# Kernel tuning notes

Hardware: AMD Instinct MI355X
Metric: run time of the kernel (lower is better)

Reference implementation:

```python
import jax, jax.numpy as jnp
from jax import lax
import numpy as np

N = 10                      # spline knots
STEP = 1.0 / (N - 1)
B, E, NC, H, W = 64, 2, 8, 256, 256

def _interp_matrix(n, step):
    # natural-cubic-spline second-derivative solve matrix (constant, numpy at trace time)
    mat = 4.0 * np.eye(n - 2)
    np.fill_diagonal(mat[1:, :-1], 1.0)
    np.fill_diagonal(mat[:-1, 1:], 1.0)
    A = 6.0 * np.linalg.inv(mat) / step ** 2
    z = np.zeros(n - 2)
    A = np.vstack([z, A, z])
    Bm = np.zeros([n - 2, n])
    np.fill_diagonal(Bm, 1.0)
    np.fill_diagonal(Bm[:, 1:], -2.0)
    np.fill_diagonal(Bm[:, 2:], 1.0)
    return (A @ Bm).astype(np.float32)

MAT = jnp.asarray(_interp_matrix(N, STEP))  # (N, N)


def setup_inputs() -> dict:
    key = jax.random.key(0)
    ks = iter(jax.random.split(key, 40))
    def w(shape, scale=0.05):
        return jax.random.normal(next(ks), shape, jnp.float32) * scale
    d = {"batch": jax.random.uniform(next(ks), (B, 3, H, W), jnp.float32)}
    chans = [3, NC, 2 * NC, 4 * NC, 8 * NC, 16 * NC]
    for i in range(1, 6):
        d[f"w{i}"] = w((chans[i], chans[i - 1], 3, 3))
        d[f"bias{i}"] = jnp.zeros((chans[i],), jnp.float32)
    for i in range(2, 6):
        c = chans[i]
        d[f"bn{i}_gamma"] = jnp.ones((c,), jnp.float32)
        d[f"bn{i}_beta"] = jnp.zeros((c,), jnp.float32)
        d[f"bn{i}_mean"] = jnp.zeros((c,), jnp.float32)
        d[f"bn{i}_var"] = jnp.ones((c,), jnp.float32)
    d["l1_w"] = w((16 * NC, 16 * NC))
    d["l1_b"] = jnp.zeros((16 * NC,), jnp.float32)
    d["l2_w"] = w((3 * N * E, 16 * NC))
    d["l2_b"] = jnp.zeros((3 * N * E,), jnp.float32)
    return d


def _conv(x, w, b):
    y = lax.conv_general_dilated(x, w, (2, 2), 'VALID',
                                 dimension_numbers=('NCHW', 'OIHW', 'NCHW'))
    return y + b[None, :, None, None]


def _bn(x, g, beta, m, v):
    s = (g * lax.rsqrt(v + 1e-5))
    return (x - m[None, :, None, None]) * s[None, :, None, None] + beta[None, :, None, None]


def _coeffs(yt):
    # yt: (B, E, 3, N) knot values (ys + identity). Returns a,b,c,d each (B,E,3,N-1).
    M = jnp.einsum('ij,becj->beci', MAT, yt)
    h = STEP
    a = (M[..., 1:] - M[..., :-1]) / (6.0 * h)
    b = M[..., :-1] / 2.0
    c = (yt[..., 1:] - yt[..., :-1]) / h - (M[..., 1:] + 2.0 * M[..., :-1]) * (h / 6.0)
    d = yt[..., :-1]
    return a, b, c, d


def _apply(a, b, c, d, xi, xf):
    # a..d: (B,E,3,N-1); xi int (B,E,3,P); xf float broadcastable to (B,E,3,P)
    ga = jnp.take_along_axis(a, xi, axis=-1)
    gb = jnp.take_along_axis(b, xi, axis=-1)
    gc = jnp.take_along_axis(c, xi, axis=-1)
    gd = jnp.take_along_axis(d, xi, axis=-1)
    return ((ga * xf + gb) * xf + gc) * xf + gd


def reference(batch, w1, bias1, w2, bias2, w3, bias3, w4, bias4, w5, bias5,
              bn2_gamma, bn2_beta, bn2_mean, bn2_var,
              bn3_gamma, bn3_beta, bn3_mean, bn3_var,
              bn4_gamma, bn4_beta, bn4_mean, bn4_var,
              bn5_gamma, bn5_beta, bn5_mean, bn5_var,
              l1_w, l1_b, l2_w, l2_b):
    y = jax.nn.relu(_conv(batch, w1, bias1))
    y = _bn(jax.nn.relu(_conv(y, w2, bias2)), bn2_gamma, bn2_beta, bn2_mean, bn2_var)
    y = _bn(jax.nn.relu(_conv(y, w3, bias3)), bn3_gamma, bn3_beta, bn3_mean, bn3_var)
    y = _bn(jax.nn.relu(_conv(y, w4, bias4)), bn4_gamma, bn4_beta, bn4_mean, bn4_var)
    y = _bn(jax.nn.relu(_conv(y, w5, bias5)), bn5_gamma, bn5_beta, bn5_mean, bn5_var)
    feat = jnp.mean(y, axis=(2, 3))                      # AvgPool2d(7) on 7x7 -> (B, 16*NC)
    hh = jax.nn.relu(feat @ l1_w.T + l1_b)
    ys = (hh @ l2_w.T + l2_b).reshape(B, E, 3, N)        # per-expert per-channel knot residuals
    identity = (jnp.arange(N, dtype=jnp.float32) / (N - 1))
    yt = ys + identity                                   # residual curves around identity
    a, b, c, d = _coeffs(yt)                             # each (B,E,3,N-1)

    # per-pixel bucketize + coefficient gather + cubic Horner eval
    P = H * W
    xv = batch.reshape(B, 3, P)
    xi = jnp.clip(jnp.floor(xv / STEP), 0, N - 2).astype(jnp.int32)
    xf = (xv - xi.astype(jnp.float32) * STEP)[:, None, :, :]       # (B,1,3,P)
    idx = jnp.broadcast_to(xi[:, None, :, :], (B, E, 3, P))
    out = _apply(a, b, c, d, idx, xf)                              # (B,E,3,P)
    out = out.reshape(B, E, 3, H, W).transpose(1, 0, 2, 3, 4)      # (E,B,3,H,W)

    # sampled spline curves over 255 uniform values
    vals = jnp.arange(0.0, 1.0, 1.0 / 255, dtype=jnp.float32)      # (255,)
    V = vals.shape[0]
    vi = jnp.clip(jnp.floor(vals / STEP), 0, N - 2).astype(jnp.int32)
    vf = vals - vi.astype(jnp.float32) * STEP
    vidx = jnp.broadcast_to(vi[None, None, None, :], (B, E, 3, V))
    splines = _apply(a, b, c, d, vidx, vf[None, None, None, :])    # (B,E,3,V)
    splines = splines.transpose(1, 0, 2, 3)                        # (E,B,3,V)
    return out, splines
```

## Files before the change

### kernel.cpp

```cpp
#include <hip/hip_runtime.h>
#include <hip/hip_bf16.h>

#define STEP_F (1.0f/9.0f)

typedef float f4 __attribute__((ext_vector_type(4)));

__global__ __launch_bounds__(256) void conv1_k(const float* __restrict__ x,
                                               const float* __restrict__ w,
                                               const float* __restrict__ bias,
                                               float* __restrict__ y)
{
    int idx = blockIdx.x * 256 + threadIdx.x;
    int owg = idx & 31;
    int t1  = idx >> 5;
    int oh  = t1 % 127;
    int b   = t1 / 127;
    int iw0 = owg * 8;
    int ih0 = oh * 2;
    const float* xb = x + (size_t)b * 3 * 65536;

    float acc[8][4];
    #pragma unroll
    for (int c = 0; c < 8; ++c)
        #pragma unroll
        for (int t = 0; t < 4; ++t) acc[c][t] = 0.0f;

    #pragma unroll
    for (int ci = 0; ci < 3; ++ci) {
        float r[3][10];
        #pragma unroll
        for (int kh = 0; kh < 3; ++kh) {
            const float* row = xb + ci * 65536 + (ih0 + kh) * 256;
            #pragma unroll
            for (int t = 0; t < 5; ++t) {
                int c = iw0 + 2 * t; if (c > 254) c = 254;
                float2 v = *(const float2*)(row + c);
                r[kh][2*t] = v.x; r[kh][2*t+1] = v.y;
            }
        }
        #pragma unroll
        for (int co = 0; co < 8; ++co) {
            float wr[9];
            #pragma unroll
            for (int k = 0; k < 9; ++k) wr[k] = w[(co * 3 + ci) * 9 + k];
            #pragma unroll
            for (int t = 0; t < 4; ++t) {
                float a = acc[co][t];
                #pragma unroll
                for (int kh = 0; kh < 3; ++kh)
                    a = fmaf(r[kh][2*t+0], wr[kh*3+0],
                        fmaf(r[kh][2*t+1], wr[kh*3+1],
                        fmaf(r[kh][2*t+2], wr[kh*3+2], a)));
                acc[co][t] = a;
            }
        }
    }
    int ow0 = owg * 4;
    #pragma unroll
    for (int co = 0; co < 8; ++co) {
        float bs = bias[co];
        float4 o;
        o.x = fmaxf(acc[co][0] + bs, 0.0f);
        o.y = fmaxf(acc[co][1] + bs, 0.0f);
        o.z = fmaxf(acc[co][2] + bs, 0.0f);
        o.w = fmaxf(acc[co][3] + bs, 0.0f);
        *(float4*)(y + (((size_t)b * 8 + co) * 127 + oh) * 128 + ow0) = o;
    }
}

__global__ __launch_bounds__(256) void conv2_k(
    const float* __restrict__ x,
    const float* __restrict__ w, const float* __restrict__ bias,
    const float* __restrict__ g, const float* __restrict__ be,
    const float* __restrict__ mn, const float* __restrict__ vr,
    float* __restrict__ y)
{
    __shared__ float lds[8 * 9 * 128 + 192];
    const int b   = blockIdx.x;
    const int ohg = blockIdx.y;
    const int oh0 = ohg * 4;
    const int ih0 = oh0 * 2;
    const int tid = threadIdx.x;

    {
        const int col = tid & 127;
        const int rp  = tid >> 7;
        const int rows = (127 - ih0) < 9 ? (127 - ih0) : 9;
        #pragma unroll
        for (int ci = 0; ci < 8; ++ci) {
            const float* gp = x + (((size_t)b * 8 + ci) * 127 + ih0) * 128 + col;
            float* lp = lds + ci * 1152 + col;
            for (int rr = rp; rr < rows; rr += 2)
                lp[rr * 128] = gp[rr * 128];
        }
    }
    __syncthreads();

    const int lane = tid & 63;
    const int wv   = __builtin_amdgcn_readfirstlane(tid >> 6);
    const int ow   = lane;
    const int co0  = wv * 4;

    float acc[4][4];
    #pragma unroll
    for (int c = 0; c < 4; ++c)
        #pragma unroll
        for (int j = 0; j < 4; ++j) acc[c][j] = 0.0f;

    #pragma unroll 2
    for (int ci = 0; ci < 8; ++ci) {
        float wr[4][9];
        #pragma unroll
        for (int c = 0; c < 4; ++c) {
            const int wb = __builtin_amdgcn_readfirstlane(((co0 + c) * 8 + ci) * 9);
            #pragma unroll
            for (int k = 0; k < 9; ++k) wr[c][k] = w[wb + k];
        }
        const float* lci = lds + ci * 1152;
        #pragma unroll
        for (int r = 0; r < 9; ++r) {
            float2 x01 = *(const float2*)&lci[r * 128 + 2 * ow];
            float  x2  = lci[r * 128 + 2 * ow + 2];
            #pragma unroll
            for (int kh = 0; kh < 3; ++kh) {
                const int jj = r - kh;
                if (jj >= 0 && (jj & 1) == 0 && (jj >> 1) < 4) {
                    const int j = jj >> 1;
                    #pragma unroll
                    for (int c = 0; c < 4; ++c)
                        acc[c][j] = fmaf(x01.x, wr[c][kh*3+0],
                                    fmaf(x01.y, wr[c][kh*3+1],
                                    fmaf(x2,    wr[c][kh*3+2], acc[c][j])));
                }
            }
        }
    }

    if (ow < 63) {
        #pragma unroll
        for (int c = 0; c < 4; ++c) {
            const int co = co0 + c;
            const float bs = bias[co];
            const float s  = g[co] / sqrtf(vr[co] + 1e-5f);
            const float sh = be[co] - mn[co] * s;
            #pragma unroll
            for (int j = 0; j < 4; ++j) {
                int oh = oh0 + j;
                if (oh < 63)
                    y[(((size_t)b * 16 + co) * 63 + oh) * 64 + ow] =
                        fmaxf(acc[c][j] + bs, 0.0f) * s + sh;
            }
        }
    }
}

__global__ __launch_bounds__(256) void conv3_k(
    const float* __restrict__ x,
    const float* __restrict__ w, const float* __restrict__ bias,
    const float* __restrict__ g, const float* __restrict__ be,
    const float* __restrict__ mn, const float* __restrict__ vr,
    float* __restrict__ y)
{
    const int b   = blockIdx.x;
    const int ohg = blockIdx.y;
    const int coh = blockIdx.z;
    const int lane = threadIdx.x & 63;
    const int wv   = __builtin_amdgcn_readfirstlane(threadIdx.x >> 6);
    const int ow   = lane & 31;
    const int ohl  = lane >> 5;
    const int co0  = coh * 16 + wv * 4;
    const int ihb  = ohg * 8 + ohl * 4;

    float acc[4][2];
    #pragma unroll
    for (int c = 0; c < 4; ++c) { acc[c][0] = 0.0f; acc[c][1] = 0.0f; }

    #pragma unroll 4
    for (int ci = 0; ci < 16; ++ci) {
        const float* gp = x + (((size_t)b * 16 + ci) * 63) * 64 + 2 * ow;
        f4 rv[5];
        #pragma unroll
        for (int r = 0; r < 5; ++r) {
            int ih = ihb + r; ih = ih > 62 ? 62 : ih;
            rv[r] = *(const f4*)(gp + ih * 64);
        }
        float wr[4][9];
        #pragma unroll
        for (int c = 0; c < 4; ++c) {
            const int wb = __builtin_amdgcn_readfirstlane(((co0 + c) * 16 + ci) * 9);
            #pragma unroll
            for (int k = 0; k < 9; ++k) wr[c][k] = w[wb + k];
        }
        #pragma unroll
        for (int j = 0; j < 2; ++j)
            #pragma unroll
            for (int kh = 0; kh < 3; ++kh) {
                const f4 v = rv[2*j + kh];
                #pragma unroll
                for (int c = 0; c < 4; ++c)
                    acc[c][j] = fmaf(v[0], wr[c][kh*3+0],
                                fmaf(v[1], wr[c][kh*3+1],
                                fmaf(v[2], wr[c][kh*3+2], acc[c][j])));
            }
    }

    if (ow < 31) {
        #pragma unroll
        for (int c = 0; c < 4; ++c) {
            const int co = co0 + c;
            const float bs = bias[co];
            const float s  = g[co] / sqrtf(vr[co] + 1e-5f);
            const float sh = be[co] - mn[co] * s;
            #pragma unroll
            for (int j = 0; j < 2; ++j) {
                int oh = ohg * 4 + ohl * 2 + j;
                if (oh < 31)
                    y[(((size_t)b * 32 + co) * 31 + oh) * 32 + ow] =
                        fmaxf(acc[c][j] + bs, 0.0f) * s + sh;
            }
        }
    }
}

__global__ __launch_bounds__(256) void conv4_k(
    const float* __restrict__ x,
    const float* __restrict__ w, const float* __restrict__ bias,
    const float* __restrict__ g, const float* __restrict__ be,
    const float* __restrict__ mn, const float* __restrict__ vr,
    float* __restrict__ y)
{
    const int b   = blockIdx.x;
    const int ohg = blockIdx.y;
    const int cog = blockIdx.z;
    const int lane = threadIdx.x & 63;
    const int wv   = __builtin_amdgcn_readfirstlane(threadIdx.x >> 6);
    const int ow   = lane & 15;
    const int ohl  = lane >> 4;
    const int oh   = ohg * 4 + ohl;
    const int co0  = cog * 16 + wv * 4;
    const int ihb  = 2 * oh;

    float acc[4];
    #pragma unroll
    for (int c = 0; c < 4; ++c) acc[c] = 0.0f;

    #pragma unroll 4
    for (int ci = 0; ci < 32; ++ci) {
        const float* gp = x + (((size_t)b * 32 + ci) * 31) * 32 + 2 * ow;
        f4 rv[3];
        #pragma unroll
        for (int r = 0; r < 3; ++r) {
            int ih = ihb + r; ih = ih > 30 ? 30 : ih;
            rv[r] = *(const f4*)(gp + ih * 32);
        }
        float wr[4][9];
        #pragma unroll
        for (int c = 0; c < 4; ++c) {
            const int wb = __builtin_amdgcn_readfirstlane(((co0 + c) * 32 + ci) * 9);
            #pragma unroll
            for (int k = 0; k < 9; ++k) wr[c][k] = w[wb + k];
        }
        #pragma unroll
        for (int kh = 0; kh < 3; ++kh) {
            const f4 v = rv[kh];
            #pragma unroll
            for (int c = 0; c < 4; ++c)
                acc[c] = fmaf(v[0], wr[c][kh*3+0],
                         fmaf(v[1], wr[c][kh*3+1],
                         fmaf(v[2], wr[c][kh*3+2], acc[c])));
        }
    }

    if (ow < 15 && oh < 15) {
        #pragma unroll
        for (int c = 0; c < 4; ++c) {
            const int co = co0 + c;
            const float bs = bias[co];
            const float s  = g[co] / sqrtf(vr[co] + 1e-5f);
            const float sh = be[co] - mn[co] * s;
            y[(((size_t)b * 64 + co) * 15 + oh) * 16 + ow] =
                fmaxf(acc[c] + bs, 0.0f) * s + sh;
        }
    }
}

__global__ __launch_bounds__(256) void conv5m_k(
    const float* __restrict__ x,
    const float* __restrict__ w, const float* __restrict__ bias,
    const float* __restrict__ g, const float* __restrict__ be,
    const float* __restrict__ mn, const float* __restrict__ vr,
    float* __restrict__ feat)
{
    __shared__ float red[2048];
    const int b    = blockIdx.x;
    const int co0  = blockIdx.y * 8;
    const int tid  = threadIdx.x;
    const int wv   = __builtin_amdgcn_readfirstlane(tid >> 6);
    const int lane = tid & 63;
    const int pr = lane >> 3, pc = lane & 7;

    float acc[8];
    #pragma unroll
    for (int c = 0; c < 8; ++c) acc[c] = 0.0f;

    #pragma unroll 4
    for (int i = 0; i < 16; ++i) {
        const int ci = wv * 16 + i;
        const float* gp = x + (((size_t)b * 64 + ci) * 15) * 16 + 2 * pc;
        f4 rv[3];
        #pragma unroll
        for (int r = 0; r < 3; ++r) {
            int ih = 2 * pr + r; ih = ih > 14 ? 14 : ih;
            rv[r] = *(const f4*)(gp + ih * 16);
        }
        float wr[8][9];
        #pragma unroll
        for (int c = 0; c < 8; ++c) {
            const int wb = __builtin_amdgcn_readfirstlane(((co0 + c) * 64 + ci) * 9);
            #pragma unroll
            for (int k = 0; k < 9; ++k) wr[c][k] = w[wb + k];
        }
        #pragma unroll
        for (int kh = 0; kh < 3; ++kh) {
            const f4 v = rv[kh];
            #pragma unroll
            for (int c = 0; c < 8; ++c)
                acc[c] = fmaf(v[0], wr[c][kh*3+0],
                         fmaf(v[1], wr[c][kh*3+1],
                         fmaf(v[2], wr[c][kh*3+2], acc[c])));
        }
    }

    #pragma unroll
    for (int c = 0; c < 8; ++c) red[wv * 512 + lane * 8 + c] = acc[c];
    __syncthreads();
    if (wv == 0) {
        const bool act = (pr < 7) && (pc < 7);
        #pragma unroll
        for (int c = 0; c < 8; ++c) {
            float v = red[lane*8+c] + red[512+lane*8+c]
                    + red[1024+lane*8+c] + red[1536+lane*8+c];
            const int co = co0 + c;
            const float s  = g[co] / sqrtf(vr[co] + 1e-5f);
            v = fmaxf(v + bias[co], 0.0f) * s + (be[co] - mn[co] * s);
            v = act ? v : 0.0f;
            #pragma unroll
            for (int off = 32; off; off >>= 1) v += __shfl_xor(v, off, 64);
            if (lane == 0) feat[(size_t)b * 128 + co] = v * (1.0f / 49.0f);
        }
    }
}

__global__ __launch_bounds__(256) void tail_k(
    const float* __restrict__ featg, const float* __restrict__ l1w,
    const float* __restrict__ l1b, const float* __restrict__ l2w,
    const float* __restrict__ l2b, float* __restrict__ coef,
    float* __restrict__ spl)
{
    __shared__ float feat[128];
    __shared__ float hh[128];
    __shared__ float ysv[64];
    __shared__ float cfl[216];
    const int b = blockIdx.x, t = threadIdx.x;

    if (t < 128) feat[t] = featg[(size_t)b * 128 + t];
    __syncthreads();
    if (t < 128) {
        const float4* wp = (const float4*)(l1w + (size_t)t * 128);
        float s = l1b[t];
        #pragma unroll 8
        for (int k = 0; k < 32; ++k) {
            float4 v = wp[k];
            s += v.x*feat[4*k] + v.y*feat[4*k+1] + v.z*feat[4*k+2] + v.w*feat[4*k+3];
        }
        hh[t] = fmaxf(s, 0.0f);
    }
    __syncthreads();
    if (t < 60) {
        const float4* wp = (const float4*)(l2w + (size_t)t * 128);
        float s = l2b[t];
        #pragma unroll 8
        for (int k = 0; k < 32; ++k) {
            float4 v = wp[k];
            s += v.x*hh[4*k] + v.y*hh[4*k+1] + v.z*hh[4*k+2] + v.w*hh[4*k+3];
        }
        ysv[t] = s;
    }
    __syncthreads();
    if (t < 6) {
        const float h = STEP_F;
        float yt[10];
        #pragma unroll
        for (int n = 0; n < 10; ++n) yt[n] = ysv[t * 10 + n] + (float)n * h;
        float r[8];
        const float k6h2 = 6.0f / (h * h);
        #pragma unroll
        for (int i = 0; i < 8; ++i) r[i] = k6h2 * (yt[i] - 2.0f * yt[i+1] + yt[i+2]);
        float cp[8], dp[8];
        cp[0] = 0.25f; dp[0] = r[0] * 0.25f;
        #pragma unroll
        for (int i = 1; i < 8; ++i) {
            float m = 4.0f - cp[i-1];
            cp[i] = 1.0f / m;
            dp[i] = (r[i] - dp[i-1]) / m;
        }
        float M[10];
        M[0] = 0.0f; M[9] = 0.0f; M[8] = dp[7];
        #pragma unroll
        for (int i = 6; i >= 0; --i) M[i+1] = dp[i] - cp[i] * M[i+2];
        float* cg = coef + ((size_t)b * 6 + t) * 36;
        #pragma unroll
        for (int i = 0; i < 9; ++i) {
            float ca = (M[i+1] - M[i]) / (6.0f * h);
            float cb = M[i] * 0.5f;
            float cc = (yt[i+1] - yt[i]) / h - (M[i+1] + 2.0f * M[i]) * (h / 6.0f);
            float cd = yt[i];
            cfl[t*36 + i]      = ca;  cg[i]      = ca;
            cfl[t*36 + 9 + i]  = cb;  cg[9 + i]  = cb;
            cfl[t*36 + 18 + i] = cc;  cg[18 + i] = cc;
            cfl[t*36 + 27 + i] = cd;  cg[27 + i] = cd;
        }
    }
    __syncthreads();
    for (int i = t; i < 1530; i += 256) {
        int v = i % 255, ec = i / 255;
        float val = (float)v * (1.0f / 255.0f);
        int vi = (int)floorf(val / STEP_F);
        vi = vi < 0 ? 0 : (vi > 8 ? 8 : vi);
        float vf = val - (float)vi * STEP_F;
        const float* c = cfl + ec * 36;
        int e = ec / 3, ch = ec % 3;
        spl[(((size_t)e * 64 + b) * 3 + ch) * 255 + v] =
            ((c[vi]*vf + c[9+vi])*vf + c[18+vi])*vf + c[27+vi];
    }
}

__global__ __launch_bounds__(256) void apply2_k(const float* __restrict__ batch,
                                                const float* __restrict__ coef,
                                                float* __restrict__ out)
{
    int bc = blockIdx.y;
    int b = bc / 3, ch = bc % 3;
    int lane = threadIdx.x & 63;
    int j = lane < 9 ? lane : 8;
    const float* c0p = coef + ((size_t)(b * 6 + 0 + ch)) * 36;
    const float* c1p = coef + ((size_t)(b * 6 + 3 + ch)) * 36;
    float A0 = c0p[j], B0 = c0p[9 + j], C0 = c0p[18 + j], D0 = c0p[27 + j];
    float A1 = c1p[j], B1 = c1p[9 + j], C1 = c1p[18 + j], D1 = c1p[27 + j];

    const int P = 65536;
    size_t base = ((size_t)b * 3 + ch) * P;
    int p0 = (blockIdx.x * blockDim.x + threadIdx.x) * 4;

    float4 xv = *(const float4*)(batch + base + p0);
    float xs[4] = {xv.x, xv.y, xv.z, xv.w};
    float r0[4], r1[4];
    #pragma unroll
    for (int k = 0; k < 4; ++k) {
        float x = xs[k];
        int xi = (int)floorf(x / STEP_F);
        xi = xi < 0 ? 0 : (xi > 8 ? 8 : xi);
        float xf = x - (float)xi * STEP_F;
        int bidx = xi << 2;
        float ga0 = __int_as_float(__builtin_amdgcn_ds_bpermute(bidx, __float_as_int(A0)));
        float gb0 = __int_as_float(__builtin_amdgcn_ds_bpermute(bidx, __float_as_int(B0)));
        float gc0 = __int_as_float(__builtin_amdgcn_ds_bpermute(bidx, __float_as_int(C0)));
        float gd0 = __int_as_float(__builtin_amdgcn_ds_bpermute(bidx, __float_as_int(D0)));
        float ga1 = __int_as_float(__builtin_amdgcn_ds_bpermute(bidx, __float_as_int(A1)));
        float gb1 = __int_as_float(__builtin_amdgcn_ds_bpermute(bidx, __float_as_int(B1)));
        float gc1 = __int_as_float(__builtin_amdgcn_ds_bpermute(bidx, __float_as_int(C1)));
        float gd1 = __int_as_float(__builtin_amdgcn_ds_bpermute(bidx, __float_as_int(D1)));
        r0[k] = fmaf(fmaf(fmaf(ga0, xf, gb0), xf, gc0), xf, gd0);
        r1[k] = fmaf(fmaf(fmaf(ga1, xf, gb1), xf, gc1), xf, gd1);
    }
    float4 o0 = {r0[0], r0[1], r0[2], r0[3]};
    float4 o1 = {r1[0], r1[1], r1[2], r1[3]};
    size_t off0 = (((size_t)0 * 64 + b) * 3 + ch) * P + p0;
    size_t off1 = (((size_t)1 * 64 + b) * 3 + ch) * P + p0;
    *(float4*)(out + off0) = o0;
    *(float4*)(out + off1) = o1;
}

extern "C" void kernel_launch(void* const* d_in, const int* in_sizes, int n_in,
                              void* d_out, int out_size, void* d_ws, size_t ws_size,
                              hipStream_t stream) {
    const float* batch = (const float*)d_in[0];
    const float* w1 = (const float*)d_in[1];  const float* b1 = (const float*)d_in[2];
    const float* w2 = (const float*)d_in[3];  const float* b2 = (const float*)d_in[4];
    const float* w3 = (const float*)d_in[5];  const float* b3 = (const float*)d_in[6];
    const float* w4 = (const float*)d_in[7];  const float* b4 = (const float*)d_in[8];
    const float* w5 = (const float*)d_in[9];  const float* b5 = (const float*)d_in[10];
    const float* bn2g = (const float*)d_in[11]; const float* bn2b = (const float*)d_in[12];
    const float* bn2m = (const float*)d_in[13]; const float* bn2v = (const float*)d_in[14];
    const float* bn3g = (const float*)d_in[15]; const float* bn3b = (const float*)d_in[16];
    const float* bn3m = (const float*)d_in[17]; const float* bn3v = (const float*)d_in[18];
    const float* bn4g = (const float*)d_in[19]; const float* bn4b = (const float*)d_in[20];
    const float* bn4m = (const float*)d_in[21]; const float* bn4v = (const float*)d_in[22];
    const float* bn5g = (const float*)d_in[23]; const float* bn5b = (const float*)d_in[24];
    const float* bn5m = (const float*)d_in[25]; const float* bn5v = (const float*)d_in[26];
    const float* l1w = (const float*)d_in[27]; const float* l1b = (const float*)d_in[28];
    const float* l2w = (const float*)d_in[29]; const float* l2b = (const float*)d_in[30];

    float* outp = (float*)d_out;
    float* y1 = outp;
    float* y2 = y1 + 8323072;
    float* y3 = y2 + 4128768;
    float* y4 = y3 + 2031616;

    float* coef  = (float*)d_ws;
    float* featw = coef + 13824;

    const int TPB = 256;
    conv1_k<<<1016, TPB, 0, stream>>>(batch, w1, b1, y1);
    conv2_k<<<dim3(64, 16), TPB, 0, stream>>>(y1, w2, b2, bn2g, bn2b, bn2m, bn2v, y2);
    conv3_k<<<dim3(64, 8, 2), TPB, 0, stream>>>(y2, w3, b3, bn3g, bn3b, bn3m, bn3v, y3);
    conv4_k<<<dim3(64, 4, 4), TPB, 0, stream>>>(y3, w4, b4, bn4g, bn4b, bn4m, bn4v, y4);
    conv5m_k<<<dim3(64, 16), TPB, 0, stream>>>(y4, w5, b5, bn5g, bn5b, bn5m, bn5v, featw);
    tail_k<<<64, TPB, 0, stream>>>(featw, l1w, l1b, l2w, l2b, coef, outp + 25165824);
    {
        dim3 grid(64, 192);
        apply2_k<<<grid, TPB, 0, stream>>>(batch, coef, outp);
    }
}
```

Baseline: 134.2 us.

## Fuse conv1 into conv2 via LDS tile and process two images per block in conv3-5

Conv1 is now computed per block directly into a shared-memory tile that conv2 consumes, removing the y1 global write and readback and one launch. Conv3, conv4 and conv5 each handle two batch images per block, halving grid size and reusing the loaded weights across both images. This trades the recomputation of overlapping conv1 halo rows and higher register pressure for lower memory traffic and fewer weight loads.

```diff
diff --git a/kernel.cpp b/kernel.cpp
--- a/kernel.cpp
+++ b/kernel.cpp
@@ -5,163 +5,146 @@
 
 typedef float f4 __attribute__((ext_vector_type(4)));
 
-__global__ __launch_bounds__(256) void conv1_k(const float* __restrict__ x,
-                                               const float* __restrict__ w,
-                                               const float* __restrict__ bias,
-                                               float* __restrict__ y)
+__global__ __launch_bounds__(256) void conv12_k(
+    const float* __restrict__ x,
+    const float* __restrict__ w1c, const float* __restrict__ b1c,
+    const float* __restrict__ w2c, const float* __restrict__ b2c,
+    const float* __restrict__ g, const float* __restrict__ be,
+    const float* __restrict__ mn, const float* __restrict__ vr,
+    float* __restrict__ y2)
 {
-    int idx = blockIdx.x * 256 + threadIdx.x;
-    int owg = idx & 31;
-    int t1  = idx >> 5;
-    int oh  = t1 % 127;
-    int b   = t1 / 127;
-    int iw0 = owg * 8;
-    int ih0 = oh * 2;
-    const float* xb = x + (size_t)b * 3 * 65536;
-
-    float acc[8][4];
-    #pragma unroll
-    for (int c = 0; c < 8; ++c)
-        #pragma unroll
-        for (int t = 0; t < 4; ++t) acc[c][t] = 0.0f;
-
-    #pragma unroll
-    for (int ci = 0; ci < 3; ++ci) {
-        float r[3][10];
-        #pragma unroll
-        for (int kh = 0; kh < 3; ++kh) {
-            const float* row = xb + ci * 65536 + (ih0 + kh) * 256;
-            #pragma unroll
-            for (int t = 0; t < 5; ++t) {
-                int c = iw0 + 2 * t; if (c > 254) c = 254;
-                float2 v = *(const float2*)(row + c);
-                r[kh][2*t] = v.x; r[kh][2*t+1] = v.y;
-            }
-        }
-        #pragma unroll
-        for (int co = 0; co < 8; ++co) {
-            float wr[9];
-            #pragma unroll
-            for (int k = 0; k < 9; ++k) wr[k] = w[(co * 3 + ci) * 9 + k];
-            #pragma unroll
-            for (int t = 0; t < 4; ++t) {
-                float a = acc[co][t];
-                #pragma unroll
-                for (int kh = 0; kh < 3; ++kh)
-                    a = fmaf(r[kh][2*t+0], wr[kh*3+0],
-                        fmaf(r[kh][2*t+1], wr[kh*3+1],
-                        fmaf(r[kh][2*t+2], wr[kh*3+2], a)));
-                acc[co][t] = a;
-            }
-        }
-    }
-    int ow0 = owg * 4;
-    #pragma unroll
-    for (int co = 0; co < 8; ++co) {
-        float bs = bias[co];
-        float4 o;
-        o.x = fmaxf(acc[co][0] + bs, 0.0f);
-        o.y = fmaxf(acc[co][1] + bs, 0.0f);
-        o.z = fmaxf(acc[co][2] + bs, 0.0f);
-        o.w = fmaxf(acc[co][3] + bs, 0.0f);
-        *(float4*)(y + (((size_t)b * 8 + co) * 127 + oh) * 128 + ow0) = o;
-    }
-}
-
-__global__ __launch_bounds__(256) void conv2_k(
+    __shared__ float y1t[8 * 1188 + 16];
+    const int b    = blockIdx.x;
+    const int ohg  = blockIdx.y;
+    const int tid  = threadIdx.x;
+    const int rows = (127 - 8 * ohg) < 9 ? (127 - 8 * ohg) : 9;
+
+    {
+        const int owg = tid & 31;
+        const int rg  = tid >> 5;
+        const float* xb = x + (size_t)b * 3 * 65536;
+        for (int r = rg; r < rows; r += 8) {
+            const int r1  = 8 * ohg + r;
+            const int ih0 = 2 * r1;
+            const int iw0 = owg * 8;
+            float acc1[8][4];
+            #pragma unroll
+            for (int c = 0; c < 8; ++c)
+                #pragma unroll
+                for (int t = 0; t < 4; ++t) acc1[c][t] = 0.0f;
+
+            #pragma unroll
+            for (int ci = 0; ci < 3; ++ci) {
+                float rr[3][10];
+                #pragma unroll
+                for (int kh = 0; kh < 3; ++kh) {
+                    const float* row = xb + ci * 65536 + (ih0 + kh) * 256;
+                    #pragma unroll
+                    for (int t = 0; t < 5; ++t) {
+                        int c = iw0 + 2 * t; if (c > 254) c = 254;
+                        float2 v = *(const float2*)(row + c);
+                        rr[kh][2*t] = v.x; rr[kh][2*t+1] = v.y;
+                    }
+                }
+                #pragma unroll
+                for (int co = 0; co < 8; ++co) {
+                    float wr[9];
+                    #pragma unroll
+                    for (int k = 0; k < 9; ++k) wr[k] = w1c[(co * 3 + ci) * 9 + k];
+                    #pragma unroll
+                    for (int t = 0; t < 4; ++t) {
+                        float a = acc1[co][t];
+                        #pragma unroll
+                        for (int kh = 0; kh < 3; ++kh)
+                            a = fmaf(rr[kh][2*t+0], wr[kh*3+0],
+                                fmaf(rr[kh][2*t+1], wr[kh*3+1],
+                                fmaf(rr[kh][2*t+2], wr[kh*3+2], a)));
+                        acc1[co][t] = a;
+                    }
+                }
+            }
+            #pragma unroll
+            for (int co = 0; co < 8; ++co) {
+                float bs = b1c[co];
+                f4 o;
+                o[0] = fmaxf(acc1[co][0] + bs, 0.0f);
+                o[1] = fmaxf(acc1[co][1] + bs, 0.0f);
+                o[2] = fmaxf(acc1[co][2] + bs, 0.0f);
+                o[3] = fmaxf(acc1[co][3] + bs, 0.0f);
+                *(f4*)&y1t[co * 1188 + r * 132 + owg * 4] = o;
+            }
+        }
+    }
+    __syncthreads();
+
+    {
+        const int lane = tid & 63;
+        const int wv   = __builtin_amdgcn_readfirstlane(tid >> 6);
+        const int ow   = lane;
+        const int co0  = wv * 4;
+
+        float acc[4][4];
+        #pragma unroll
+        for (int c = 0; c < 4; ++c)
+            #pragma unroll
+            for (int j = 0; j < 4; ++j) acc[c][j] = 0.0f;
+
+        #pragma unroll 2
+        for (int ci = 0; ci < 8; ++ci) {
+            float wr[4][9];
+            #pragma unroll
+            for (int c = 0; c < 4; ++c) {
+                const int wb = __builtin_amdgcn_readfirstlane(((co0 + c) * 8 + ci) * 9);
+                #pragma unroll
+                for (int k = 0; k < 9; ++k) wr[c][k] = w2c[wb + k];
+            }
+            const float* lci = y1t + ci * 1188;
+            #pragma unroll
+            for (int r = 0; r < 9; ++r) {
+                float2 x01 = *(const float2*)&lci[r * 132 + 2 * ow];
+                float  x2  = lci[r * 132 + 2 * ow + 2];
+                #pragma unroll
+                for (int kh = 0; kh < 3; ++kh) {
+                    const int jj = r - kh;
+                    if (jj >= 0 && (jj & 1) == 0 && (jj >> 1) < 4) {
+                        const int j = jj >> 1;
+                        #pragma unroll
+                        for (int c = 0; c < 4; ++c)
+                            acc[c][j] = fmaf(x01.x, wr[c][kh*3+0],
+                                        fmaf(x01.y, wr[c][kh*3+1],
+                                        fmaf(x2,    wr[c][kh*3+2], acc[c][j])));
+                    }
+                }
+            }
+        }
+
+        if (ow < 63) {
+            #pragma unroll
+            for (int c = 0; c < 4; ++c) {
+                const int co = co0 + c;
+                const float bs = b2c[co];
+                const float s  = g[co] / sqrtf(vr[co] + 1e-5f);
+                const float sh = be[co] - mn[co] * s;
+                #pragma unroll
+                for (int j = 0; j < 4; ++j) {
+                    int oh = 4 * ohg + j;
+                    if (oh < 63)
+                        y2[(((size_t)b * 16 + co) * 63 + oh) * 64 + ow] =
+                            fmaxf(acc[c][j] + bs, 0.0f) * s + sh;
+                }
+            }
+        }
+    }
+}
+
+__global__ __launch_bounds__(256) void conv3b_k(
     const float* __restrict__ x,
     const float* __restrict__ w, const float* __restrict__ bias,
     const float* __restrict__ g, const float* __restrict__ be,
     const float* __restrict__ mn, const float* __restrict__ vr,
     float* __restrict__ y)
 {
-    __shared__ float lds[8 * 9 * 128 + 192];
-    const int b   = blockIdx.x;
-    const int ohg = blockIdx.y;
-    const int oh0 = ohg * 4;
-    const int ih0 = oh0 * 2;
-    const int tid = threadIdx.x;
-
-    {
-        const int col = tid & 127;
-        const int rp  = tid >> 7;
-        const int rows = (127 - ih0) < 9 ? (127 - ih0) : 9;
-        #pragma unroll
-        for (int ci = 0; ci < 8; ++ci) {
-            const float* gp = x + (((size_t)b * 8 + ci) * 127 + ih0) * 128 + col;
-            float* lp = lds + ci * 1152 + col;
-            for (int rr = rp; rr < rows; rr += 2)
-                lp[rr * 128] = gp[rr * 128];
-        }
-    }
-    __syncthreads();
-
-    const int lane = tid & 63;
-    const int wv   = __builtin_amdgcn_readfirstlane(tid >> 6);
-    const int ow   = lane;
-    const int co0  = wv * 4;
-
-    float acc[4][4];
-    #pragma unroll
-    for (int c = 0; c < 4; ++c)
-        #pragma unroll
-        for (int j = 0; j < 4; ++j) acc[c][j] = 0.0f;
-
-    #pragma unroll 2
-    for (int ci = 0; ci < 8; ++ci) {
-        float wr[4][9];
-        #pragma unroll
-        for (int c = 0; c < 4; ++c) {
-            const int wb = __builtin_amdgcn_readfirstlane(((co0 + c) * 8 + ci) * 9);
-            #pragma unroll
-            for (int k = 0; k < 9; ++k) wr[c][k] = w[wb + k];
-        }
-        const float* lci = lds + ci * 1152;
-        #pragma unroll
-        for (int r = 0; r < 9; ++r) {
-            float2 x01 = *(const float2*)&lci[r * 128 + 2 * ow];
-            float  x2  = lci[r * 128 + 2 * ow + 2];
-            #pragma unroll
-            for (int kh = 0; kh < 3; ++kh) {
-                const int jj = r - kh;
-                if (jj >= 0 && (jj & 1) == 0 && (jj >> 1) < 4) {
-                    const int j = jj >> 1;
-                    #pragma unroll
-                    for (int c = 0; c < 4; ++c)
-                        acc[c][j] = fmaf(x01.x, wr[c][kh*3+0],
-                                    fmaf(x01.y, wr[c][kh*3+1],
-                                    fmaf(x2,    wr[c][kh*3+2], acc[c][j])));
-                }
-            }
-        }
-    }
-
-    if (ow < 63) {
-        #pragma unroll
-        for (int c = 0; c < 4; ++c) {
-            const int co = co0 + c;
-            const float bs = bias[co];
-            const float s  = g[co] / sqrtf(vr[co] + 1e-5f);
-            const float sh = be[co] - mn[co] * s;
-            #pragma unroll
-            for (int j = 0; j < 4; ++j) {
-                int oh = oh0 + j;
-                if (oh < 63)
-                    y[(((size_t)b * 16 + co) * 63 + oh) * 64 + ow] =
-                        fmaxf(acc[c][j] + bs, 0.0f) * s + sh;
-            }
-        }
-    }
-}
-
-__global__ __launch_bounds__(256) void conv3_k(
-    const float* __restrict__ x,
-    const float* __restrict__ w, const float* __restrict__ bias,
-    const float* __restrict__ g, const float* __restrict__ be,
-    const float* __restrict__ mn, const float* __restrict__ vr,
-    float* __restrict__ y)
-{
-    const int b   = blockIdx.x;
+    const int b0  = blockIdx.x, b1 = b0 + 32;
     const int ohg = blockIdx.y;
     const int coh = blockIdx.z;
     const int lane = threadIdx.x & 63;
@@ -171,18 +154,22 @@
     const int co0  = coh * 16 + wv * 4;
     const int ihb  = ohg * 8 + ohl * 4;
 
-    float acc[4][2];
+    float acc[2][4][2];
     #pragma unroll
-    for (int c = 0; c < 4; ++c) { acc[c][0] = 0.0f; acc[c][1] = 0.0f; }
-
-    #pragma unroll 4
+    for (int p = 0; p < 2; ++p)
+        #pragma unroll
+        for (int c = 0; c < 4; ++c) { acc[p][c][0] = 0.0f; acc[p][c][1] = 0.0f; }
+
+    #pragma unroll 2
     for (int ci = 0; ci < 16; ++ci) {
-        const float* gp = x + (((size_t)b * 16 + ci) * 63) * 64 + 2 * ow;
-        f4 rv[5];
+        const float* gp0 = x + (((size_t)b0 * 16 + ci) * 63) * 64 + 2 * ow;
+        const float* gp1 = x + (((size_t)b1 * 16 + ci) * 63) * 64 + 2 * ow;
+        f4 rv0[5], rv1[5];
         #pragma unroll
         for (int r = 0; r < 5; ++r) {
             int ih = ihb + r; ih = ih > 62 ? 62 : ih;
-            rv[r] = *(const f4*)(gp + ih * 64);
+            rv0[r] = *(const f4*)(gp0 + ih * 64);
+            rv1[r] = *(const f4*)(gp1 + ih * 64);
         }
         float wr[4][9];
         #pragma unroll
@@ -195,12 +182,17 @@
         for (int j = 0; j < 2; ++j)
             #pragma unroll
             for (int kh = 0; kh < 3; ++kh) {
-                const f4 v = rv[2*j + kh];
-                #pragma unroll
-                for (int c = 0; c < 4; ++c)
-                    acc[c][j] = fmaf(v[0], wr[c][kh*3+0],
-                                fmaf(v[1], wr[c][kh*3+1],
-                                fmaf(v[2], wr[c][kh*3+2], acc[c][j])));
+                const f4 v0 = rv0[2*j + kh];
+                const f4 v1 = rv1[2*j + kh];
+                #pragma unroll
+                for (int c = 0; c < 4; ++c) {
+                    acc[0][c][j] = fmaf(v0[0], wr[c][kh*3+0],
+                                   fmaf(v0[1], wr[c][kh*3+1],
+                                   fmaf(v0[2], wr[c][kh*3+2], acc[0][c][j])));
+                    acc[1][c][j] = fmaf(v1[0], wr[c][kh*3+0],
+                                   fmaf(v1[1], wr[c][kh*3+1],
+                                   fmaf(v1[2], wr[c][kh*3+2], acc[1][c][j])));
+                }
             }
     }
 
@@ -214,22 +206,25 @@
             #pragma unroll
             for (int j = 0; j < 2; ++j) {
                 int oh = ohg * 4 + ohl * 2 + j;
-                if (oh < 31)
-                    y[(((size_t)b * 32 + co) * 31 + oh) * 32 + ow] =
-                        fmaxf(acc[c][j] + bs, 0.0f) * s + sh;
-            }
-        }
-    }
-}
-
-__global__ __launch_bounds__(256) void conv4_k(
+                if (oh < 31) {
+                    y[(((size_t)b0 * 32 + co) * 31 + oh) * 32 + ow] =
+                        fmaxf(acc[0][c][j] + bs, 0.0f) * s + sh;
+                    y[(((size_t)b1 * 32 + co) * 31 + oh) * 32 + ow] =
+                        fmaxf(acc[1][c][j] + bs, 0.0f) * s + sh;
+                }
+            }
+        }
+    }
+}
+
+__global__ __launch_bounds__(256) void conv4b_k(
     const float* __restrict__ x,
     const float* __restrict__ w, const float* __restrict__ bias,
     const float* __restrict__ g, const float* __restrict__ be,
     const float* __restrict__ mn, const float* __restrict__ vr,
     float* __restrict__ y)
 {
-    const int b   = blockIdx.x;
+    const int b0  = blockIdx.x, b1 = b0 + 32;
     const int ohg = blockIdx.y;
     const int cog = blockIdx.z;
     const int lane = threadIdx.x & 63;
@@ -240,18 +235,22 @@
     const int co0  = cog * 16 + wv * 4;
     const int ihb  = 2 * oh;
 
-    float acc[4];
+    float acc[2][4];
     #pragma unroll
-    for (int c = 0; c < 4; ++c) acc[c] = 0.0f;
+    for (int p = 0; p < 2; ++p)
+        #pragma unroll
+        for (int c = 0; c < 4; ++c) acc[p][c] = 0.0f;
 
     #pragma unroll 4
     for (int ci = 0; ci < 32; ++ci) {
-        const float* gp = x + (((size_t)b * 32 + ci) * 31) * 32 + 2 * ow;
-        f4 rv[3];
+        const float* gp0 = x + (((size_t)b0 * 32 + ci) * 31) * 32 + 2 * ow;
+        const float* gp1 = x + (((size_t)b1 * 32 + ci) * 31) * 32 + 2 * ow;
+        f4 rv0[3], rv1[3];
         #pragma unroll
         for (int r = 0; r < 3; ++r) {
             int ih = ihb + r; ih = ih > 30 ? 30 : ih;
-            rv[r] = *(const f4*)(gp + ih * 32);
+            rv0[r] = *(const f4*)(gp0 + ih * 32);
+            rv1[r] = *(const f4*)(gp1 + ih * 32);
         }
         float wr[4][9];
         #pragma unroll
@@ -262,12 +261,17 @@
         }
         #pragma unroll
         for (int kh = 0; kh < 3; ++kh) {
-            const f4 v = rv[kh];
-            #pragma unroll
-            for (int c = 0; c < 4; ++c)
-                acc[c] = fmaf(v[0], wr[c][kh*3+0],
-                         fmaf(v[1], wr[c][kh*3+1],
-                         fmaf(v[2], wr[c][kh*3+2], acc[c])));
+            const f4 v0 = rv0[kh];
+            const f4 v1 = rv1[kh];
+            #pragma unroll
+            for (int c = 0; c < 4; ++c) {
+                acc[0][c] = fmaf(v0[0], wr[c][kh*3+0],
+                            fmaf(v0[1], wr[c][kh*3+1],
+                            fmaf(v0[2], wr[c][kh*3+2], acc[0][c])));
+                acc[1][c] = fmaf(v1[0], wr[c][kh*3+0],
+                            fmaf(v1[1], wr[c][kh*3+1],
+                            fmaf(v1[2], wr[c][kh*3+2], acc[1][c])));
+            }
         }
     }
 
@@ -278,40 +282,44 @@
             const float bs = bias[co];
             const float s  = g[co] / sqrtf(vr[co] + 1e-5f);
             const float sh = be[co] - mn[co] * s;
-            y[(((size_t)b * 64 + co) * 15 + oh) * 16 + ow] =
-                fmaxf(acc[c] + bs, 0.0f) * s + sh;
-        }
-    }
-}
-
-__global__ __launch_bounds__(256) void conv5m_k(
+            y[(((size_t)b0 * 64 + co) * 15 + oh) * 16 + ow] =
+                fmaxf(acc[0][c] + bs, 0.0f) * s + sh;
+            y[(((size_t)b1 * 64 + co) * 15 + oh) * 16 + ow] =
+                fmaxf(acc[1][c] + bs, 0.0f) * s + sh;
+        }
+    }
+}
+
+__global__ __launch_bounds__(256) void conv5m2_k(
     const float* __restrict__ x,
     const float* __restrict__ w, const float* __restrict__ bias,
     const float* __restrict__ g, const float* __restrict__ be,
     const float* __restrict__ mn, const float* __restrict__ vr,
     float* __restrict__ feat)
 {
-    __shared__ float red[2048];
-    const int b    = blockIdx.x;
+    __shared__ float red[2 * 2304 + 32];
+    const int b0   = blockIdx.x, b1 = b0 + 32;
     const int co0  = blockIdx.y * 8;
     const int tid  = threadIdx.x;
     const int wv   = __builtin_amdgcn_readfirstlane(tid >> 6);
     const int lane = tid & 63;
     const int pr = lane >> 3, pc = lane & 7;
 
-    float acc[8];
+    float a0[8], a1[8];
     #pragma unroll
-    for (int c = 0; c < 8; ++c) acc[c] = 0.0f;
+    for (int c = 0; c < 8; ++c) { a0[c] = 0.0f; a1[c] = 0.0f; }
 
     #pragma unroll 4
     for (int i = 0; i < 16; ++i) {
         const int ci = wv * 16 + i;
-        const float* gp = x + (((size_t)b * 64 + ci) * 15) * 16 + 2 * pc;
-        f4 rv[3];
+        const float* gp0 = x + (((size_t)b0 * 64 + ci) * 15) * 16 + 2 * pc;
+        const float* gp1 = x + (((size_t)b1 * 64 + ci) * 15) * 16 + 2 * pc;
+        f4 rv0[3], rv1[3];
         #pragma unroll
         for (int r = 0; r < 3; ++r) {
             int ih = 2 * pr + r; ih = ih > 14 ? 14 : ih;
-            rv[r] = *(const f4*)(gp + ih * 16);
+            rv0[r] = *(const f4*)(gp0 + ih * 16);
+            rv1[r] = *(const f4*)(gp1 + ih * 16);
         }
         float wr[8][9];
         #pragma unroll
@@ -322,31 +330,41 @@
         }
         #pragma unroll
         for (int kh = 0; kh < 3; ++kh) {
-            const f4 v = rv[kh];
-            #pragma unroll
-            for (int c = 0; c < 8; ++c)
-                acc[c] = fmaf(v[0], wr[c][kh*3+0],
-                         fmaf(v[1], wr[c][kh*3+1],
-                         fmaf(v[2], wr[c][kh*3+2], acc[c])));
+            const f4 v0 = rv0[kh];
+            const f4 v1 = rv1[kh];
+            #pragma unroll
+            for (int c = 0; c < 8; ++c) {
+                a0[c] = fmaf(v0[0], wr[c][kh*3+0],
+                        fmaf(v0[1], wr[c][kh*3+1],
+                        fmaf(v0[2], wr[c][kh*3+2], a0[c])));
+                a1[c] = fmaf(v1[0], wr[c][kh*3+0],
+                        fmaf(v1[1], wr[c][kh*3+1],
+                        fmaf(v1[2], wr[c][kh*3+2], a1[c])));
+            }
         }
     }
 
     #pragma unroll
-    for (int c = 0; c < 8; ++c) red[wv * 512 + lane * 8 + c] = acc[c];
+    for (int c = 0; c < 8; ++c) {
+        red[0 * 2304 + wv * 576 + lane * 9 + c] = a0[c];
+        red[1 * 2304 + wv * 576 + lane * 9 + c] = a1[c];
+    }
     __syncthreads();
-    if (wv == 0) {
+    if (wv < 2) {
+        const int base = wv * 2304;
+        const int bb   = wv ? b1 : b0;
         const bool act = (pr < 7) && (pc < 7);
         #pragma unroll
         for (int c = 0; c < 8; ++c) {
-            float v = red[lane*8+c] + red[512+lane*8+c]
-                    + red[1024+lane*8+c] + red[1536+lane*8+c];
+            float v = red[base + 0*576 + lane*9 + c] + red[base + 1*576 + lane*9 + c]
+                    + red[base + 2*576 + lane*9 + c] + red[base + 3*576 + lane*9 + c];
             const int co = co0 + c;
-            const float s  = g[co] / sqrtf(vr[co] + 1e-5f);
+            const float s = g[co] / sqrtf(vr[co] + 1e-5f);
             v = fmaxf(v + bias[co], 0.0f) * s + (be[co] - mn[co] * s);
             v = act ? v : 0.0f;
             #pragma unroll
             for (int off = 32; off; off >>= 1) v += __shfl_xor(v, off, 64);
-            if (lane == 0) feat[(size_t)b * 128 + co] = v * (1.0f / 49.0f);
+            if (lane == 0) feat[(size_t)bb * 128 + co] = v * (1.0f / 49.0f);
         }
     }
 }
@@ -502,8 +520,7 @@
     const float* l2w = (const float*)d_in[29]; const float* l2b = (const float*)d_in[30];
 
     float* outp = (float*)d_out;
-    float* y1 = outp;
-    float* y2 = y1 + 8323072;
+    float* y2 = outp;
     float* y3 = y2 + 4128768;
     float* y4 = y3 + 2031616;
 
@@ -511,11 +528,11 @@
     float* featw = coef + 13824;
 
     const int TPB = 256;
-    conv1_k<<<1016, TPB, 0, stream>>>(batch, w1, b1, y1);
-    conv2_k<<<dim3(64, 16), TPB, 0, stream>>>(y1, w2, b2, bn2g, bn2b, bn2m, bn2v, y2);
-    conv3_k<<<dim3(64, 8, 2), TPB, 0, stream>>>(y2, w3, b3, bn3g, bn3b, bn3m, bn3v, y3);
-    conv4_k<<<dim3(64, 4, 4), TPB, 0, stream>>>(y3, w4, b4, bn4g, bn4b, bn4m, bn4v, y4);
-    conv5m_k<<<dim3(64, 16), TPB, 0, stream>>>(y4, w5, b5, bn5g, bn5b, bn5m, bn5v, featw);
+    conv12_k<<<dim3(64, 16), TPB, 0, stream>>>(batch, w1, b1, w2, b2,
+                                               bn2g, bn2b, bn2m, bn2v, y2);
+    conv3b_k<<<dim3(32, 8, 2), TPB, 0, stream>>>(y2, w3, b3, bn3g, bn3b, bn3m, bn3v, y3);
+    conv4b_k<<<dim3(32, 4, 4), TPB, 0, stream>>>(y3, w4, b4, bn4g, bn4b, bn4m, bn4v, y4);
+    conv5m2_k<<<dim3(32, 16), TPB, 0, stream>>>(y4, w5, b5, bn5g, bn5b, bn5m, bn5v, featw);
     tail_k<<<64, TPB, 0, stream>>>(featw, l1w, l1b, l2w, l2b, coef, outp + 25165824);
     {
         dim3 grid(64, 192);
```

Measured after the change: 136.9 us. 1.02x slower.

## Reorder conv grids so batch is outermost and stage conv5 weights in LDS

Applied to the files above, without the earlier changes.

Conv2-4 grids are flattened so blocks that share one batch image are launched next to each other, which should improve L2 locality of activation reads. Conv5 now cooperatively loads its 8-output-channel weight slice into LDS once per block, instead of reading weights through scalar global loads on every iteration. The reduction buffer is padded to a stride of 9 to avoid LDS bank conflicts, and the unroll factor drops to 2. The cost is extra LDS use (about 27KB), which may limit occupancy, and an up-front weight load with a barrier.

```diff
diff --git a/kernel.cpp b/kernel.cpp
--- a/kernel.cpp
+++ b/kernel.cpp
@@ -76,8 +76,8 @@
     float* __restrict__ y)
 {
     __shared__ float lds[8 * 9 * 128 + 192];
-    const int b   = blockIdx.x;
-    const int ohg = blockIdx.y;
+    const int ohg = blockIdx.x;
+    const int b   = blockIdx.y;
     const int oh0 = ohg * 4;
     const int ih0 = oh0 * 2;
     const int tid = threadIdx.x;
@@ -161,9 +161,9 @@
     const float* __restrict__ mn, const float* __restrict__ vr,
     float* __restrict__ y)
 {
-    const int b   = blockIdx.x;
-    const int ohg = blockIdx.y;
-    const int coh = blockIdx.z;
+    const int ohg = blockIdx.x & 7;
+    const int coh = blockIdx.x >> 3;
+    const int b   = blockIdx.y;
     const int lane = threadIdx.x & 63;
     const int wv   = __builtin_amdgcn_readfirstlane(threadIdx.x >> 6);
     const int ow   = lane & 31;
@@ -229,9 +229,9 @@
     const float* __restrict__ mn, const float* __restrict__ vr,
     float* __restrict__ y)
 {
-    const int b   = blockIdx.x;
-    const int ohg = blockIdx.y;
-    const int cog = blockIdx.z;
+    const int ohg = blockIdx.x & 3;
+    const int cog = blockIdx.x >> 2;
+    const int b   = blockIdx.y;
     const int lane = threadIdx.x & 63;
     const int wv   = __builtin_amdgcn_readfirstlane(threadIdx.x >> 6);
     const int ow   = lane & 15;
@@ -284,17 +284,25 @@
     }
 }
 
-__global__ __launch_bounds__(256) void conv5m_k(
+__global__ __launch_bounds__(256) void conv5w_k(
     const float* __restrict__ x,
     const float* __restrict__ w, const float* __restrict__ bias,
     const float* __restrict__ g, const float* __restrict__ be,
     const float* __restrict__ mn, const float* __restrict__ vr,
     float* __restrict__ feat)
 {
-    __shared__ float red[2048];
-    const int b    = blockIdx.x;
-    const int co0  = blockIdx.y * 8;
+    __shared__ float lw[4608];
+    __shared__ float red[4 * 580 + 16];
+    const int co0  = blockIdx.x * 8;
+    const int b    = blockIdx.y;
     const int tid  = threadIdx.x;
+
+    {
+        const float* wp = w + (size_t)co0 * 576;
+        for (int i = tid; i < 4608; i += 256) lw[i] = wp[i];
+    }
+    __syncthreads();
+
     const int wv   = __builtin_amdgcn_readfirstlane(tid >> 6);
     const int lane = tid & 63;
     const int pr = lane >> 3, pc = lane & 7;
@@ -303,7 +311,7 @@
     #pragma unroll
     for (int c = 0; c < 8; ++c) acc[c] = 0.0f;
 
-    #pragma unroll 4
+    #pragma unroll 2
     for (int i = 0; i < 16; ++i) {
         const int ci = wv * 16 + i;
         const float* gp = x + (((size_t)b * 64 + ci) * 15) * 16 + 2 * pc;
@@ -316,9 +324,9 @@
         float wr[8][9];
         #pragma unroll
         for (int c = 0; c < 8; ++c) {
-            const int wb = __builtin_amdgcn_readfirstlane(((co0 + c) * 64 + ci) * 9);
-            #pragma unroll
-            for (int k = 0; k < 9; ++k) wr[c][k] = w[wb + k];
+            const float* lwp = lw + (c * 64 + ci) * 9;
+            #pragma unroll
+            for (int k = 0; k < 9; ++k) wr[c][k] = lwp[k];
         }
         #pragma unroll
         for (int kh = 0; kh < 3; ++kh) {
@@ -332,16 +340,16 @@
     }
 
     #pragma unroll
-    for (int c = 0; c < 8; ++c) red[wv * 512 + lane * 8 + c] = acc[c];
+    for (int c = 0; c < 8; ++c) red[wv * 580 + lane * 9 + c] = acc[c];
     __syncthreads();
     if (wv == 0) {
         const bool act = (pr < 7) && (pc < 7);
         #pragma unroll
         for (int c = 0; c < 8; ++c) {
-            float v = red[lane*8+c] + red[512+lane*8+c]
-                    + red[1024+lane*8+c] + red[1536+lane*8+c];
+            float v = red[lane*9+c] + red[580+lane*9+c]
+                    + red[1160+lane*9+c] + red[1740+lane*9+c];
             const int co = co0 + c;
-            const float s  = g[co] / sqrtf(vr[co] + 1e-5f);
+            const float s = g[co] / sqrtf(vr[co] + 1e-5f);
             v = fmaxf(v + bias[co], 0.0f) * s + (be[co] - mn[co] * s);
             v = act ? v : 0.0f;
             #pragma unroll
@@ -509,14 +517,15 @@
 
     float* coef  = (float*)d_ws;
     float* featw = coef + 13824;
+    float* spl   = outp + 25165824;
 
     const int TPB = 256;
     conv1_k<<<1016, TPB, 0, stream>>>(batch, w1, b1, y1);
-    conv2_k<<<dim3(64, 16), TPB, 0, stream>>>(y1, w2, b2, bn2g, bn2b, bn2m, bn2v, y2);
-    conv3_k<<<dim3(64, 8, 2), TPB, 0, stream>>>(y2, w3, b3, bn3g, bn3b, bn3m, bn3v, y3);
-    conv4_k<<<dim3(64, 4, 4), TPB, 0, stream>>>(y3, w4, b4, bn4g, bn4b, bn4m, bn4v, y4);
-    conv5m_k<<<dim3(64, 16), TPB, 0, stream>>>(y4, w5, b5, bn5g, bn5b, bn5m, bn5v, featw);
-    tail_k<<<64, TPB, 0, stream>>>(featw, l1w, l1b, l2w, l2b, coef, outp + 25165824);
+    conv2_k<<<dim3(16, 64), TPB, 0, stream>>>(y1, w2, b2, bn2g, bn2b, bn2m, bn2v, y2);
+    conv3_k<<<dim3(16, 64), TPB, 0, stream>>>(y2, w3, b3, bn3g, bn3b, bn3m, bn3v, y3);
+    conv4_k<<<dim3(16, 64), TPB, 0, stream>>>(y3, w4, b4, bn4g, bn4b, bn4m, bn4v, y4);
+    conv5w_k<<<dim3(16, 64), TPB, 0, stream>>>(y4, w5, b5, bn5g, bn5b, bn5m, bn5v, featw);
+    tail_k<<<64, TPB, 0, stream>>>(featw, l1w, l1b, l2w, l2b, coef, spl);
     {
         dim3 grid(64, 192);
         apply2_k<<<grid, TPB, 0, stream>>>(batch, coef, outp);
```

Result: no change. 133.6 us (-0.4%).
